# Kernel optimization log

Hardware: AMD Instinct MI355X
Metric: run time of the kernel (lower is better)

The kernel has to match this reference:

```python
import math
import jax, jax.numpy as jnp
import numpy as np
from jax import lax

B, T, D, S, N_SLOTS, N_ITERS = 16, 4096, 768, 768, 16, 8
THR, EPS = 0.5, 1e-8
SCALE = D ** -0.5
NEG = -jnp.finfo(jnp.float32).max


def ln(x, g, b):
    mu = x.mean(-1, keepdims=True)
    var = ((x - mu) ** 2).mean(-1, keepdims=True)
    return (x - mu) / jnp.sqrt(var + 1e-5) * g + b


def gru_cell(u, h, wih, whh, bih, bhh):
    # torch GRUCell: r,z,n gate ordering
    gi = u @ wih.T + bih
    gh = h @ whh.T + bhh
    ir, iz, inn = jnp.split(gi, 3, axis=-1)
    hr, hz, hn = jnp.split(gh, 3, axis=-1)
    r = jax.nn.sigmoid(ir + hr)
    z = jax.nn.sigmoid(iz + hz)
    n = jnp.tanh(inn + r * hn)
    return (1.0 - z) * n + z * h


def sa_step(slots, k, v, p, slot_mask, context_mask):
    q = ln(slots, p['lsg'], p['lsb']) @ p['Wq'].T
    dots = jnp.einsum('bid,bjd->bij', q, k) * SCALE  # [B, n_slots, T]
    dots = jnp.where(context_mask[:, None, :], dots, NEG)
    if slot_mask is not None:
        dots = jnp.where(slot_mask[:, :, None], dots, NEG)
    attn_vis = jax.nn.softmax(dots, axis=1)  # softmax over SLOTS (inverted attn)
    attn = attn_vis + EPS
    attn = attn / attn.sum(-1, keepdims=True)
    updates = jnp.einsum('bjd,bij->bid', v, attn)
    b, n, d = slots.shape
    h = gru_cell(updates.reshape(b * n, d), slots.reshape(b * n, d),
                 p['gwih'], p['gwhh'], p['gbih'], p['gbhh'])
    slots = h.reshape(b, n, d)
    pre = ln(slots, p['lfg'], p['lfb'])
    slots = slots + (jax.nn.relu(pre @ p['w1'].T + p['b1']) @ p['w2'].T + p['b2'])
    return slots, attn_vis


def cluster_single(slots, attn, slot_mask):
    sl = lax.stop_gradient(slots)  # torch no_grad block
    ns = sl / jnp.clip(jnp.linalg.norm(sl, axis=-1, keepdims=True), 1e-12)
    smm = (slot_mask[:, :, None] & slot_mask[:, None, :]).astype(jnp.float32)
    dist = 1.0 - jnp.einsum('bnd,bmd->bnm', ns, ns)
    dist = jnp.where(smm > 0, dist, 2.0)
    adj = (dist < THR).astype(jnp.float32) * smm
    for _ in range(math.ceil(math.log2(N_SLOTS))):  # transitive closure by squaring
        adj = jnp.minimum(adj @ adj, 1.0) * smm
    cum = jnp.cumsum(adj, axis=1)
    cm = adj * (cum <= 1.0)  # keep first row of each connected component
    counts = (cm > 0).any(axis=2).sum(axis=1)
    reset = counts < 3
    eye = jnp.eye(N_SLOTS, dtype=jnp.float32)[None] * slot_mask[:, :, None].astype(jnp.float32)
    cm = jnp.where(reset[:, None, None], eye, cm)
    cw = cm / jnp.clip(cm.sum(axis=2, keepdims=True), 1.0)
    cm = lax.stop_gradient(cm)
    cw = lax.stop_gradient(cw)
    means = cw @ slots          # grads flow through slots only
    cattn = cm @ attn           # grads flow through attn only
    out_mask = (cm > 0).any(axis=2) & slot_mask
    return means, cattn, out_mask


def setup_inputs() -> dict:
    key = jax.random.key(0)
    ks = jax.random.split(key, 16)
    sc = 0.02
    return {
        'x': jax.random.normal(ks[0], (B, T, D), jnp.float32),
        'context_mask': jnp.ones((B, T), jnp.bool_),
        'n_slots': N_SLOTS,
        'slots_init': jax.random.normal(ks[1], (N_SLOTS, S), jnp.float32),
        'Wk': jax.random.normal(ks[2], (S, D), jnp.float32) * sc,
        'Wv': jax.random.normal(ks[3], (S, D), jnp.float32) * sc,
        'Wq': jax.random.normal(ks[4], (S, S), jnp.float32) * sc,
        'gwih': jax.random.normal(ks[5], (3 * S, S), jnp.float32) * sc,
        'gwhh': jax.random.normal(ks[6], (3 * S, S), jnp.float32) * sc,
        'gbih': jnp.zeros((3 * S,), jnp.float32),
        'gbhh': jnp.zeros((3 * S,), jnp.float32),
        'w1': jax.random.normal(ks[7], (4 * S, S), jnp.float32) * sc,
        'b1': jnp.zeros((4 * S,), jnp.float32),
        'w2': jax.random.normal(ks[8], (S, 4 * S), jnp.float32) * sc,
        'b2': jnp.zeros((S,), jnp.float32),
        'lin_g': jnp.ones((D,), jnp.float32), 'lin_b': jnp.zeros((D,), jnp.float32),
        'lsg': jnp.ones((S,), jnp.float32), 'lsb': jnp.zeros((S,), jnp.float32),
        'lfg': jnp.ones((S,), jnp.float32), 'lfb': jnp.zeros((S,), jnp.float32),
    }


def reference(x, context_mask, n_slots, slots_init, Wk, Wv, Wq, gwih, gwhh,
              gbih, gbhh, w1, b1, w2, b2, lin_g, lin_b, lsg, lsb, lfg, lfb):
    p = dict(Wq=Wq, gwih=gwih, gwhh=gwhh, gbih=gbih, gbhh=gbhh,
             w1=w1, b1=b1, w2=w2, b2=b2, lsg=lsg, lsb=lsb, lfg=lfg, lfb=lfb)
    xn = ln(x, lin_g, lin_b)
    init_slots = jnp.broadcast_to(slots_init[None], (x.shape[0], N_SLOTS, S))
    k = xn @ Wk.T
    v = xn @ Wv.T
    slots = init_slots
    for _ in range(N_ITERS):
        slots, attn = sa_step(slots, k, v, p, None, context_mask)
    # implicit differentiation trick
    slots = lax.stop_gradient(slots) - lax.stop_gradient(init_slots) + init_slots
    slot_mask = jnp.ones((x.shape[0], N_SLOTS), jnp.bool_)
    slots, attn = sa_step(slots, k, v, p, slot_mask, context_mask)
    slots, attn, slot_mask = cluster_single(slots, attn, slot_mask)
    attn_map = jnp.transpose(attn, (0, 2, 1))  # [B, T, n_slots]
    return slots, attn_map, slot_mask
```

## Files before the change

kernel.cpp:

```cpp
#include <hip/hip_runtime.h>
#include <hip/hip_bf16.h>

typedef __hip_bfloat16 bf16;
typedef __attribute__((ext_vector_type(4))) float f32x4;
typedef __attribute__((ext_vector_type(8))) short s16x8;
typedef unsigned int u32;
typedef unsigned short u16;

#define B_ 16
#define T_ 4096
#define D_ 768
#define S_ 768
#define NS 16
#define NIT 9
#define NCHUNK 16
#define TCH 256
#define EPS 1e-8f
#define SCALE 0.036084391824351615f

__device__ __forceinline__ void gld16(const void* g, void* l) {
    __builtin_amdgcn_global_load_lds((const __attribute__((address_space(1))) u32*)g,
                                     (__attribute__((address_space(3))) u32*)l, 16, 0, 0);
}

__device__ __forceinline__ u16 bfbits(float x) {
    bf16 h = __float2bfloat16(x);
    return *reinterpret_cast<u16*>(&h);
}

__global__ void __launch_bounds__(256) cvt_all_kernel(
    const float* __restrict__ wq, const float* __restrict__ wk, const float* __restrict__ wv,
    const float* __restrict__ gwih, const float* __restrict__ gwhh,
    const float* __restrict__ w1, const float* __restrict__ w2,
    bf16* __restrict__ wq_b, bf16* __restrict__ wkv_b,
    bf16* __restrict__ gwih_b, bf16* __restrict__ gwhh_b,
    bf16* __restrict__ w1_b, bf16* __restrict__ w2_b)
{
    int i = blockIdx.x * 256 + threadIdx.x;
    const int NW = 589824, NG = 1769472, NM = 2359296;
    if (i < NW) { wq_b[i] = __float2bfloat16(wq[i]); return; }
    i -= NW;
    if (i < NW) { wkv_b[i] = __float2bfloat16(wk[i]); return; }
    i -= NW;
    if (i < NW) { wkv_b[NW + i] = __float2bfloat16(wv[i]); return; }
    i -= NW;
    if (i < NG) { gwih_b[i] = __float2bfloat16(gwih[i]); return; }
    i -= NG;
    if (i < NG) { gwhh_b[i] = __float2bfloat16(gwhh[i]); return; }
    i -= NG;
    if (i < NM) { w1_b[i] = __float2bfloat16(w1[i]); return; }
    i -= NM;
    w2_b[i] = __float2bfloat16(w2[i]);
}

__global__ void __launch_bounds__(256) ln768_kernel(
    const float* __restrict__ x, const float* __restrict__ g,
    const float* __restrict__ bta, bf16* __restrict__ out)
{
    int row = blockIdx.x;
    int tid = threadIdx.x;
    const float* xr = x + (size_t)row * 768;
    float v0 = xr[tid], v1 = xr[tid + 256], v2 = xr[tid + 512];
    float s = v0 + v1 + v2;
    int lane = tid & 63, wid = tid >> 6;
    #pragma unroll
    for (int off = 32; off; off >>= 1) s += __shfl_down(s, off);
    __shared__ float red[4];
    __shared__ float sh_mu, sh_rs;
    if (lane == 0) red[wid] = s;
    __syncthreads();
    if (tid == 0) sh_mu = (red[0] + red[1] + red[2] + red[3]) * (1.f / 768.f);
    __syncthreads();
    float mu = sh_mu;
    float d0 = v0 - mu, d1 = v1 - mu, d2 = v2 - mu;
    float q = d0 * d0 + d1 * d1 + d2 * d2;
    #pragma unroll
    for (int off = 32; off; off >>= 1) q += __shfl_down(q, off);
    if (lane == 0) red[wid] = q;
    __syncthreads();
    if (tid == 0) sh_rs = rsqrtf((red[0] + red[1] + red[2] + red[3]) * (1.f / 768.f) + 1e-5f);
    __syncthreads();
    float rs = sh_rs;
    bf16* orow = out + (size_t)row * 768;
    orow[tid]       = __float2bfloat16(d0 * rs * g[tid]       + bta[tid]);
    orow[tid + 256] = __float2bfloat16(d1 * rs * g[tid + 256] + bta[tid + 256]);
    orow[tid + 512] = __float2bfloat16(d2 * rs * g[tid + 512] + bta[tid + 512]);
}

__global__ void __launch_bounds__(512) gemm256_kernel(
    const bf16* __restrict__ A, const bf16* __restrict__ W,
    bf16* __restrict__ kout, bf16* __restrict__ vTout, float* __restrict__ vsum)
{
    __shared__ char smem[49152];
    __shared__ float vs_l[128];
    bf16* As = (bf16*)smem;
    bf16* Bs = (bf16*)(smem + 32768);
    int tid = threadIdx.x, lane = tid & 63, wid = tid >> 6;
    int bid = blockIdx.x;
    int xcd = bid & 7, idx = bid >> 3;
    int mt = xcd * 32 + idx / 12;
    int nt = idx % 12;
    int bm0 = mt * 256, bn0 = nt * 128;
    int wr = wid >> 1, wc = wid & 1;
    int g = lane >> 4, r15 = lane & 15;
    const f32x4 vzero = {0.f, 0.f, 0.f, 0.f};
    f32x4 acc[4][4];
    #pragma unroll
    for (int m = 0; m < 4; ++m)
        #pragma unroll
        for (int n = 0; n < 4; ++n) acc[m][n] = vzero;

    for (int kt = 0; kt < 768; kt += 64) {
        __syncthreads();
        #pragma unroll
        for (int i = 0; i < 4; ++i) {
            int s0 = i * 512 + wid * 64;
            int o = (s0 + lane) * 16;
            int r = o >> 7, cb = o & 127;
            int cbs = cb ^ ((r & 7) << 4);
            gld16(A + (size_t)(bm0 + r) * 768 + kt + (cbs >> 1), (char*)As + (size_t)s0 * 16);
        }
        #pragma unroll
        for (int i = 0; i < 2; ++i) {
            int s0 = i * 512 + wid * 64;
            int o = (s0 + lane) * 16;
            int r = o >> 7, cb = o & 127;
            int cbs = cb ^ ((r & 7) << 4);
            gld16(W + (size_t)(bn0 + r) * 768 + kt + (cbs >> 1), (char*)Bs + (size_t)s0 * 16);
        }
        asm volatile("s_waitcnt vmcnt(0)" ::: "memory");
        __syncthreads();
        #pragma unroll
        for (int kk2 = 0; kk2 < 2; ++kk2) {
            s16x8 af[4], bfr[4];
            #pragma unroll
            for (int m = 0; m < 4; ++m) {
                int r = wr * 64 + m * 16 + r15;
                int p = r * 128 + ((kk2 * 64 + g * 16) ^ ((r & 7) << 4));
                af[m] = *(const s16x8*)((const char*)As + p);
            }
            #pragma unroll
            for (int n = 0; n < 4; ++n) {
                int r = wc * 64 + n * 16 + r15;
                int p = r * 128 + ((kk2 * 64 + g * 16) ^ ((r & 7) << 4));
                bfr[n] = *(const s16x8*)((const char*)Bs + p);
            }
            #pragma unroll
            for (int m = 0; m < 4; ++m)
                #pragma unroll
                for (int n = 0; n < 4; ++n)
                    acc[m][n] = __builtin_amdgcn_mfma_f32_16x16x32_bf16(af[m], bfr[n], acc[m][n], 0, 0, 0);
        }
    }

    bool is_v = (bn0 >= 768);
    float* Ct = (float*)smem;
    int bq = bm0 >> 12;
    int tloc = bm0 & 4095;
    if (is_v && tid < 128) vs_l[tid] = 0.f;
    #pragma unroll
    for (int q = 0; q < 4; ++q) {
        __syncthreads();
        if (wr == q) {
            #pragma unroll
            for (int m = 0; m < 4; ++m)
                #pragma unroll
                for (int n = 0; n < 4; ++n)
                    #pragma unroll
                    for (int j = 0; j < 4; ++j)
                        Ct[(m * 16 + g * 4 + j) * 132 + wc * 64 + n * 16 + r15] = acc[m][n][j];
        }
        __syncthreads();
        if (!is_v) {
            int r = tid >> 3, cq = tid & 7;
            u16 tmp[16];
            #pragma unroll
            for (int i = 0; i < 16; ++i) tmp[i] = bfbits(Ct[r * 132 + cq * 16 + i]);
            s16x8 o0, o1;
            #pragma unroll
            for (int i = 0; i < 8; ++i) { o0[i] = (short)tmp[i]; o1[i] = (short)tmp[8 + i]; }
            bf16* dst = kout + (size_t)(bm0 + q * 64 + r) * 768 + bn0 + cq * 16;
            *(s16x8*)dst = o0;
            *(s16x8*)(dst + 8) = o1;
        } else {
            int d = tid >> 2, tq = tid & 3;
            float ssum = 0.f;
            u16 tmp[16];
            #pragma unroll
            for (int i = 0; i < 16; ++i) {
                float f = Ct[(tq * 16 + i) * 132 + d];
                ssum += f;
                tmp[i] = bfbits(f);
            }
            s16x8 o0, o1;
            #pragma unroll
            for (int i = 0; i < 8; ++i) { o0[i] = (short)tmp[i]; o1[i] = (short)tmp[8 + i]; }
            bf16* dst = vTout + ((size_t)bq * 768 + (bn0 - 768) + d) * (size_t)T_
                        + tloc + q * 64 + tq * 16;
            *(s16x8*)dst = o0;
            *(s16x8*)(dst + 8) = o1;
            atomicAdd(&vs_l[d], ssum);
        }
    }
    if (is_v) {
        __syncthreads();
        if (tid < 128) atomicAdd(vsum + bq * 768 + (bn0 - 768) + tid, vs_l[tid]);
    }
}

__global__ void init_slots_kernel(const float* __restrict__ si,
                                  float* __restrict__ slots, bf16* __restrict__ slots_bf)
{
    int idx = blockIdx.x * 256 + threadIdx.x;
    float v = si[idx % (NS * S_)];
    slots[idx] = v;
    slots_bf[idx] = __float2bfloat16(v);
}

__global__ void __launch_bounds__(256) ln_gemm_kernel(
    const float* __restrict__ xin, const float* __restrict__ gam, const float* __restrict__ bet,
    const bf16* __restrict__ W, const float* __restrict__ bias,
    bf16* __restrict__ out, int N, int relu)
{
    __shared__ bf16 As[16 * 768];
    __shared__ bf16 Ws[2][64 * 64];
    int tid = threadIdx.x;
    int bx = blockIdx.x, bn0 = blockIdx.y * 64;
    int row = tid >> 4, li = tid & 15;
    const float* xr = xin + (size_t)(bx * 16 + row) * 768;
    float vals[48];
    float s = 0.f;
    #pragma unroll
    for (int i = 0; i < 48; ++i) { vals[i] = xr[li + i * 16]; s += vals[i]; }
    #pragma unroll
    for (int m = 1; m < 16; m <<= 1) s += __shfl_xor(s, m);
    float mu = s * (1.f / 768.f);
    float q = 0.f;
    #pragma unroll
    for (int i = 0; i < 48; ++i) { float d = vals[i] - mu; q += d * d; }
    #pragma unroll
    for (int m = 1; m < 16; m <<= 1) q += __shfl_xor(q, m);
    float rs = rsqrtf(q * (1.f / 768.f) + 1e-5f);
    #pragma unroll
    for (int i = 0; i < 48; ++i) {
        int c = li + i * 16;
        float v = (vals[i] - mu) * rs * gam[c] + bet[c];
        *(u16*)((char*)As + row * 1536 + ((c * 2) ^ ((row & 7) << 4))) = bfbits(v);
    }
    int lane = tid & 63, wid = tid >> 6;
    int g = lane >> 4, s15 = lane & 15;
    auto stageW = [&](int kt, int buf) {
        #pragma unroll
        for (int i = 0; i < 2; ++i) {
            int s0 = i * 256 + wid * 64;
            int o = (s0 + lane) * 16;
            int r = o >> 7, cb = o & 127;
            int cbs = cb ^ ((r & 7) << 4);
            gld16(W + (size_t)(bn0 + r) * 768 + kt + (cbs >> 1),
                  (char*)Ws[buf] + (size_t)s0 * 16);
        }
    };
    stageW(0, 0);
    asm volatile("s_waitcnt vmcnt(0)" ::: "memory");
    __syncthreads();
    f32x4 acc = {0.f, 0.f, 0.f, 0.f};
    int rb = wid * 16 + s15;
    for (int t = 0; t < 12; ++t) {
        int cur = t & 1;
        if (t < 11) stageW((t + 1) * 64, cur ^ 1);
        #pragma unroll
        for (int kk2 = 0; kk2 < 2; ++kk2) {
            int kabs = t * 64 + kk2 * 32;
            s16x8 af = *(const s16x8*)((const char*)As + s15 * 1536 +
                                       ((kabs * 2 + g * 16) ^ ((s15 & 7) << 4)));
            s16x8 bf_ = *(const s16x8*)((const char*)Ws[cur] + rb * 128 +
                                        ((kk2 * 64 + g * 16) ^ ((rb & 7) << 4)));
            acc = __builtin_amdgcn_mfma_f32_16x16x32_bf16(af, bf_, acc, 0, 0, 0);
        }
        asm volatile("s_waitcnt vmcnt(0)" ::: "memory");
        __syncthreads();
    }
    int cn = bn0 + rb;
    float bv = bias ? bias[cn] : 0.f;
    #pragma unroll
    for (int j = 0; j < 4; ++j) {
        float val = acc[j] + bv;
        if (relu) val = fmaxf(val, 0.f);
        out[(size_t)(bx * 16 + g * 4 + j) * N + cn] = __float2bfloat16(val);
    }
}

__device__ __forceinline__ void skinny_body(
    const bf16* A, const bf16* Bm, const float* bias, const float* Cin,
    float* Cf, bf16* Cb, int N, int K, int bm0, int bn0, int relu,
    bf16* As, bf16* Bs)
{
    int tid = threadIdx.x, lane = tid & 63, wid = tid >> 6;
    int g = lane >> 4, r15 = lane & 15;
    f32x4 acc = {0.f, 0.f, 0.f, 0.f};
    for (int kt = 0; kt < K; kt += 64) {
        __syncthreads();
        #pragma unroll
        for (int i = 0; i < 3; ++i) {
            int s0 = i * 256 + wid * 64;
            if (s0 < 640) {
                int o = (s0 + lane) * 16;
                if (o < 2048) {
                    int r = o >> 7, cb = o & 127;
                    int cbs = cb ^ ((r & 7) << 4);
                    gld16(A + (size_t)(bm0 + r) * K + kt + (cbs >> 1), (char*)As + (size_t)s0 * 16);
                } else {
                    int ob = o - 2048;
                    int r = ob >> 7, cb = ob & 127;
                    int cbs = cb ^ ((r & 7) << 4);
                    gld16(Bm + (size_t)(bn0 + r) * K + kt + (cbs >> 1),
                          (char*)Bs + (size_t)(s0 * 16 - 2048));
                }
            }
        }
        asm volatile("s_waitcnt vmcnt(0)" ::: "memory");
        __syncthreads();
        #pragma unroll
        for (int kk = 0; kk < 64; kk += 32) {
            int pa = r15 * 128 + ((kk * 2 + g * 16) ^ ((r15 & 7) << 4));
            s16x8 af = *(const s16x8*)((const char*)As + pa);
            int rb = wid * 16 + r15;
            int pb = rb * 128 + ((kk * 2 + g * 16) ^ ((rb & 7) << 4));
            s16x8 bfr = *(const s16x8*)((const char*)Bs + pb);
            acc = __builtin_amdgcn_mfma_f32_16x16x32_bf16(af, bfr, acc, 0, 0, 0);
        }
    }
    int cn = bn0 + wid * 16 + r15;
    float bv = bias ? bias[cn] : 0.f;
    #pragma unroll
    for (int j = 0; j < 4; ++j) {
        int cm = bm0 + g * 4 + j;
        size_t ci = (size_t)cm * N + cn;
        float val = acc[j] + bv;
        if (Cin) val += Cin[ci];
        if (relu) val = fmaxf(val, 0.f);
        if (Cf) Cf[ci] = val;
        if (Cb) Cb[ci] = __float2bfloat16(val);
    }
}

__global__ void __launch_bounds__(256) mlp2_kernel(
    const bf16* __restrict__ h1, const bf16* __restrict__ W2, const float* __restrict__ b2,
    const float* __restrict__ slotsB, float* __restrict__ slotsA, bf16* __restrict__ slotsA_bf)
{
    __shared__ bf16 As[16 * 64];
    __shared__ bf16 Bs[64 * 64];
    skinny_body(h1, W2, b2, slotsB, slotsA, slotsA_bf, 768, 3072,
                blockIdx.x * 16, blockIdx.y * 64, 0, As, Bs);
}

__global__ void __launch_bounds__(256) gru_gemm_kernel(
    const bf16* __restrict__ upd, const bf16* __restrict__ slots_bf,
    const bf16* __restrict__ Wih, const bf16* __restrict__ Whh,
    const float* __restrict__ bih, const float* __restrict__ bhh,
    float* __restrict__ gi, float* __restrict__ gh)
{
    __shared__ bf16 As[16 * 64];
    __shared__ bf16 Bs[64 * 64];
    int y = blockIdx.y;
    if (y < 36)
        skinny_body(upd, Wih, bih, nullptr, gi, nullptr, 2304, 768,
                    blockIdx.x * 16, y * 64, 0, As, Bs);
    else
        skinny_body(slots_bf, Whh, bhh, nullptr, gh, nullptr, 2304, 768,
                    blockIdx.x * 16, (y - 36) * 64, 0, As, Bs);
}

__global__ void __launch_bounds__(256) fused_attn_kernel(
    const bf16* __restrict__ q_bf, const bf16* __restrict__ k_bf, const bf16* __restrict__ vT,
    float* __restrict__ pU, float* __restrict__ prs, float* __restrict__ avis, int write_avis)
{
    __shared__ char smem[131072];
    bf16* ks0 = (bf16*)smem;
    bf16* ks1 = (bf16*)(smem + 49152);
    bf16* qs  = (bf16*)(smem + 98304);
    char* aL  = smem + 122880;
    __shared__ float rsw[2][16];
    int tid = threadIdx.x, lane = tid & 63, wid = tid >> 6;
    int b = blockIdx.x >> 4, chunk = blockIdx.x & 15;
    int t0 = chunk * TCH;
    int g = lane >> 4, s15 = lane & 15;
    const bf16* qb  = q_bf + (size_t)b * 16 * 768;
    const bf16* kb  = k_bf + (size_t)b * T_ * 768;
    const bf16* vtb = vT + (size_t)b * 768 * T_;

    auto stage_k = [&](int tb, bf16* dst) {
        #pragma unroll
        for (int i = 0; i < 12; ++i) {
            int s0 = i * 256 + wid * 64;
            int o = (s0 + lane) * 16;
            int r = o / 1536, cb = o % 1536;
            int cbs = cb ^ ((r & 7) << 4);
            gld16(kb + (size_t)(tb + r) * 768 + (cbs >> 1), (char*)dst + (size_t)s0 * 16);
        }
    };
    auto stage_v = [&](int tb, bf16* dst) {
        #pragma unroll
        for (int i = 0; i < 12; ++i) {
            int s0 = i * 256 + wid * 64;
            int o = (s0 + lane) * 16;
            int d = o >> 6, cb = o & 63;
            int cbs = cb ^ ((d & 3) << 4);
            gld16(vtb + (size_t)d * T_ + tb + (cbs >> 1), (char*)dst + (size_t)s0 * 16);
        }
    };

    #pragma unroll
    for (int i = 0; i < 6; ++i) {
        int s0 = i * 256 + wid * 64;
        int o = (s0 + lane) * 16;
        int r = o / 1536, cb = o % 1536;
        int cbs = cb ^ ((r & 7) << 4);
        gld16(qb + (size_t)r * 768 + (cbs >> 1), (char*)qs + (size_t)s0 * 16);
    }
    stage_k(t0, ks0);
    asm volatile("s_waitcnt vmcnt(0)" ::: "memory");
    __syncthreads();

    const f32x4 vzero = {0.f, 0.f, 0.f, 0.f};
    float rs_acc = 0.f;

    for (int ts = 0; ts < 8; ++ts) {
        bf16* cur = (ts & 1) ? ks1 : ks0;
        bf16* nxt = (ts & 1) ? ks0 : ks1;
        if (ts < 7) stage_k(t0 + (ts + 1) * 32, nxt);
        if (wid < 2) {
            f32x4 dacc = vzero;
            #pragma unroll
            for (int kk = 0; kk < 768; kk += 32) {
                int rk = wid * 16 + s15;
                int pk = rk * 1536 + ((kk * 2 + g * 16) ^ ((rk & 7) << 4));
                s16x8 kf = *(const s16x8*)((const char*)cur + pk);
                int pq = s15 * 1536 + ((kk * 2 + g * 16) ^ ((s15 & 7) << 4));
                s16x8 qf = *(const s16x8*)((const char*)qs + pq);
                dacc = __builtin_amdgcn_mfma_f32_16x16x32_bf16(kf, qf, dacc, 0, 0, 0);
            }
            float d0 = dacc[0] * SCALE, d1 = dacc[1] * SCALE,
                  d2 = dacc[2] * SCALE, d3 = dacc[3] * SCALE;
            float m0 = d0, m1 = d1, m2 = d2, m3 = d3;
            #pragma unroll
            for (int off = 1; off < 16; off <<= 1) {
                m0 = fmaxf(m0, __shfl_xor(m0, off));
                m1 = fmaxf(m1, __shfl_xor(m1, off));
                m2 = fmaxf(m2, __shfl_xor(m2, off));
                m3 = fmaxf(m3, __shfl_xor(m3, off));
            }
            float e0 = expf(d0 - m0), e1 = expf(d1 - m1), e2 = expf(d2 - m2), e3 = expf(d3 - m3);
            float q0 = e0, q1 = e1, q2 = e2, q3 = e3;
            #pragma unroll
            for (int off = 1; off < 16; off <<= 1) {
                q0 += __shfl_xor(q0, off);
                q1 += __shfl_xor(q1, off);
                q2 += __shfl_xor(q2, off);
                q3 += __shfl_xor(q3, off);
            }
            float a0 = e0 / q0, a1 = e1 / q1, a2 = e2 / q2, a3 = e3 / q3;
            rs_acc += a0 + a1 + a2 + a3;
            int tl = wid * 16 + g * 4;
            ushort2 p0, p1;
            p0.x = bfbits(a0); p0.y = bfbits(a1);
            p1.x = bfbits(a2); p1.y = bfbits(a3);
            int sw = (s15 & 3) << 4;
            char* aS = aL + ts * 1024;
            *(ushort2*)(aS + s15 * 64 + ((tl * 2) ^ sw))       = p0;
            *(ushort2*)(aS + s15 * 64 + (((tl + 2) * 2) ^ sw)) = p1;
            if (write_avis) {
                f32x4 w = {a0, a1, a2, a3};
                *(f32x4*)(avis + (size_t)(b * 16 + s15) * T_ + t0 + ts * 32 + tl) = w;
            }
        }
        asm volatile("s_waitcnt vmcnt(0)" ::: "memory");
        __syncthreads();
    }

    f32x4 uacc[12];
    #pragma unroll
    for (int i = 0; i < 12; ++i) uacc[i] = vzero;
    stage_v(t0, ks0);
    asm volatile("s_waitcnt vmcnt(0)" ::: "memory");
    __syncthreads();
    for (int ts = 0; ts < 8; ++ts) {
        bf16* cur = (ts & 1) ? ks1 : ks0;
        bf16* nxt = (ts & 1) ? ks0 : ks1;
        if (ts < 7) stage_v(t0 + (ts + 1) * 32, nxt);
        {
            int pa = ts * 1024 + s15 * 64 + ((g * 16) ^ ((s15 & 3) << 4));
            s16x8 afr = *(const s16x8*)(aL + pa);
            #pragma unroll
            for (int i = 0; i < 12; ++i) {
                int d = (wid * 12 + i) * 16 + s15;
                int pv = d * 64 + ((g * 16) ^ ((d & 3) << 4));
                s16x8 vf = *(const s16x8*)((const char*)cur + pv);
                uacc[i] = __builtin_amdgcn_mfma_f32_16x16x32_bf16(vf, afr, uacc[i], 0, 0, 0);
            }
        }
        asm volatile("s_waitcnt vmcnt(0)" ::: "memory");
        __syncthreads();
    }

    float* pUb = pU + (size_t)(b * 16 + chunk) * 768 * 16;
    #pragma unroll
    for (int i = 0; i < 12; ++i) {
        int dbase = (wid * 12 + i) * 16 + g * 4;
        #pragma unroll
        for (int j = 0; j < 4; ++j)
            pUb[(size_t)(dbase + j) * 16 + s15] = uacc[i][j];
    }
    rs_acc += __shfl_xor(rs_acc, 16);
    rs_acc += __shfl_xor(rs_acc, 32);
    if (wid < 2 && lane < 16) rsw[wid][s15] = rs_acc;
    __syncthreads();
    if (tid < 16) prs[(b * 16 + chunk) * 16 + tid] = rsw[0][tid] + rsw[1][tid];
}

__global__ void __launch_bounds__(256) attn_reduce_kernel(
    const float* __restrict__ pU, const float* __restrict__ prs,
    const float* __restrict__ vsum, bf16* __restrict__ upd)
{
    int idx = blockIdx.x * 256 + threadIdx.x;
    int d = idx % 768;
    int s = (idx / 768) & 15;
    int b = idx / (768 * 16);
    float su = 0.f;
    #pragma unroll
    for (int c = 0; c < 16; ++c) su += pU[((size_t)(b * 16 + c) * 768 + d) * 16 + s];
    float rs = 0.f;
    #pragma unroll
    for (int c = 0; c < 16; ++c) rs += prs[(b * 16 + c) * 16 + s];
    float val = (su + EPS * vsum[b * 768 + d]) / (rs + T_ * EPS);
    upd[idx] = __float2bfloat16(val);
}

__global__ void __launch_bounds__(256) gru_gates_kernel(
    const float* __restrict__ gi, const float* __restrict__ gh,
    const float* __restrict__ slotsA, float* __restrict__ slotsB)
{
    int idx = blockIdx.x * 256 + threadIdx.x;
    int r = idx / 768, c = idx - r * 768;
    const float* gir = gi + (size_t)r * 2304;
    const float* ghr = gh + (size_t)r * 2304;
    float ir = gir[c], iz = gir[768 + c], inn = gir[1536 + c];
    float hr = ghr[c], hz = ghr[768 + c], hn  = ghr[1536 + c];
    float rg = 1.f / (1.f + expf(-(ir + hr)));
    float z  = 1.f / (1.f + expf(-(iz + hz)));
    float n  = tanhf(inn + rg * hn);
    float h  = slotsA[idx];
    slotsB[idx] = (1.f - z) * n + z * h;
}

__global__ void __launch_bounds__(256) cluster_kernel(
    const float* __restrict__ slots, float* __restrict__ out_slots,
    float* __restrict__ out_mask, float* __restrict__ cm_g)
{
    int b = blockIdx.x;
    __shared__ float s[16][768];
    __shared__ float inv[16];
    __shared__ float adj[16][16], tmp[16][16], cw[16][16];
    __shared__ int reset_s;
    const float* sb = slots + (size_t)b * 16 * 768;
    for (int i = threadIdx.x; i < 16 * 768; i += 256) s[i / 768][i % 768] = sb[i];
    __syncthreads();
    if (threadIdx.x < 16) {
        float q = 0.f;
        for (int d = 0; d < 768; ++d) q += s[threadIdx.x][d] * s[threadIdx.x][d];
        inv[threadIdx.x] = 1.f / fmaxf(sqrtf(q), 1e-12f);
    }
    __syncthreads();
    int n = threadIdx.x >> 4, m = threadIdx.x & 15;
    float dot = 0.f;
    for (int d = 0; d < 768; ++d) dot += s[n][d] * s[m][d];
    dot *= inv[n] * inv[m];
    adj[n][m] = ((1.f - dot) < 0.5f) ? 1.f : 0.f;
    __syncthreads();
    #pragma unroll
    for (int it = 0; it < 4; ++it) {
        float t = 0.f;
        #pragma unroll
        for (int j = 0; j < 16; ++j) t += adj[n][j] * adj[j][m];
        tmp[n][m] = fminf(t, 1.f);
        __syncthreads();
        adj[n][m] = tmp[n][m];
        __syncthreads();
    }
    if (threadIdx.x < 16) {
        int mm = threadIdx.x;
        float run = 0.f;
        for (int nn = 0; nn < 16; ++nn) {
            run += adj[nn][mm];
            tmp[nn][mm] = adj[nn][mm] * ((run <= 1.f) ? 1.f : 0.f);
        }
    }
    __syncthreads();
    if (threadIdx.x == 0) {
        int cnt = 0;
        for (int nn = 0; nn < 16; ++nn) {
            bool any = false;
            for (int j = 0; j < 16; ++j) any = any || (tmp[nn][j] > 0.f);
            cnt += any ? 1 : 0;
        }
        reset_s = (cnt < 3) ? 1 : 0;
    }
    __syncthreads();
    if (reset_s) tmp[n][m] = (n == m) ? 1.f : 0.f;
    __syncthreads();
    if (threadIdx.x < 16) {
        float rs = 0.f;
        for (int j = 0; j < 16; ++j) rs += tmp[threadIdx.x][j];
        rs = fmaxf(rs, 1.f);
        for (int j = 0; j < 16; ++j) cw[threadIdx.x][j] = tmp[threadIdx.x][j] / rs;
        bool any = false;
        for (int j = 0; j < 16; ++j) any = any || (tmp[threadIdx.x][j] > 0.f);
        out_mask[b * 16 + threadIdx.x] = any ? 1.f : 0.f;
    }
    cm_g[b * 256 + threadIdx.x] = tmp[n][m];
    __syncthreads();
    for (int i = threadIdx.x; i < 16 * 768; i += 256) {
        int nn = i / 768, d = i - nn * 768;
        float acc = 0.f;
        #pragma unroll
        for (int j = 0; j < 16; ++j) acc += cw[nn][j] * s[j][d];
        out_slots[(size_t)b * 16 * 768 + i] = acc;
    }
}

__global__ void __launch_bounds__(256) cattn_kernel(
    const float* __restrict__ av, const float* __restrict__ cm_g, float* __restrict__ out_attn)
{
    int b = blockIdx.y;
    int t = blockIdx.x * 256 + threadIdx.x;
    __shared__ float cm[16][16];
    cm[threadIdx.x >> 4][threadIdx.x & 15] = cm_g[b * 256 + threadIdx.x];
    __syncthreads();
    float avv[16];
    #pragma unroll
    for (int j = 0; j < 16; ++j) avv[j] = av[((size_t)b * 16 + j) * T_ + t];
    #pragma unroll
    for (int i = 0; i < 16; ++i) {
        float acc = 0.f;
        #pragma unroll
        for (int j = 0; j < 16; ++j) acc += cm[i][j] * avv[j];
        out_attn[((size_t)b * T_ + t) * 16 + i] = acc;
    }
}

extern "C" void kernel_launch(void* const* d_in, const int* in_sizes, int n_in,
                              void* d_out, int out_size, void* d_ws, size_t ws_size,
                              hipStream_t stream)
{
    const float* x    = (const float*)d_in[0];
    const float* si   = (const float*)d_in[3];
    const float* Wk   = (const float*)d_in[4];
    const float* Wv   = (const float*)d_in[5];
    const float* Wq   = (const float*)d_in[6];
    const float* gwih = (const float*)d_in[7];
    const float* gwhh = (const float*)d_in[8];
    const float* gbih = (const float*)d_in[9];
    const float* gbhh = (const float*)d_in[10];
    const float* w1   = (const float*)d_in[11];
    const float* b1   = (const float*)d_in[12];
    const float* w2   = (const float*)d_in[13];
    const float* b2   = (const float*)d_in[14];
    const float* ling = (const float*)d_in[15];
    const float* linb = (const float*)d_in[16];
    const float* lsg  = (const float*)d_in[17];
    const float* lsb  = (const float*)d_in[18];
    const float* lfg  = (const float*)d_in[19];
    const float* lfb  = (const float*)d_in[20];

    char* w = (char*)d_ws;
    size_t off = 0;
    auto alloc = [&](size_t bytes) { void* p = w + off; off += (bytes + 255) & ~(size_t)255; return p; };
    bf16* xn     = (bf16*)alloc((size_t)B_ * T_ * D_ * 2);
    bf16* k_bf   = (bf16*)alloc((size_t)B_ * T_ * S_ * 2);
    bf16* vT     = (bf16*)alloc((size_t)B_ * S_ * T_ * 2);
    float* avis  = (float*)alloc((size_t)B_ * NS * T_ * 4);
    float* pU    = (float*)alloc((size_t)B_ * NCHUNK * S_ * NS * 4);
    float* prs   = (float*)alloc((size_t)B_ * NCHUNK * NS * 4);
    float* vsum  = (float*)alloc((size_t)B_ * S_ * 4);
    float* slotsA = (float*)alloc((size_t)B_ * NS * S_ * 4);
    bf16* slotsA_bf = (bf16*)alloc((size_t)B_ * NS * S_ * 2);
    float* slotsB = (float*)alloc((size_t)B_ * NS * S_ * 4);
    bf16* q_bf   = (bf16*)alloc((size_t)B_ * NS * S_ * 2);
    bf16* upd_bf = (bf16*)alloc((size_t)B_ * NS * S_ * 2);
    float* gi    = (float*)alloc((size_t)B_ * NS * 3 * S_ * 4);
    float* gh    = (float*)alloc((size_t)B_ * NS * 3 * S_ * 4);
    bf16* h1_bf  = (bf16*)alloc((size_t)B_ * NS * 4 * S_ * 2);
    bf16* wq_bf  = (bf16*)alloc((size_t)S_ * S_ * 2);
    bf16* wkv_bf = (bf16*)alloc((size_t)1536 * D_ * 2);
    bf16* gwih_bf = (bf16*)alloc((size_t)3 * S_ * S_ * 2);
    bf16* gwhh_bf = (bf16*)alloc((size_t)3 * S_ * S_ * 2);
    bf16* w1_bf  = (bf16*)alloc((size_t)4 * S_ * S_ * 2);
    bf16* w2_bf  = (bf16*)alloc((size_t)S_ * 4 * S_ * 2);
    float* cm_g  = (float*)alloc((size_t)B_ * 256 * 4);

    float* out_slots = (float*)d_out;
    float* out_attn  = out_slots + (size_t)B_ * NS * S_;
    float* out_mask  = out_attn + (size_t)B_ * T_ * NS;

    cvt_all_kernel<<<39168, 256, 0, stream>>>(Wq, Wk, Wv, gwih, gwhh, w1, w2,
                                              wq_bf, wkv_bf, gwih_bf, gwhh_bf, w1_bf, w2_bf);

    ln768_kernel<<<B_ * T_, 256, 0, stream>>>(x, ling, linb, xn);

    (void)hipMemsetAsync(vsum, 0, (size_t)B_ * S_ * 4, stream);
    gemm256_kernel<<<3072, 512, 0, stream>>>(xn, wkv_bf, k_bf, vT, vsum);

    init_slots_kernel<<<(B_ * NS * S_) / 256, 256, 0, stream>>>(si, slotsA, slotsA_bf);

    for (int it = 0; it < NIT; ++it) {
        {
            dim3 g(16, 12);
            ln_gemm_kernel<<<g, 256, 0, stream>>>(slotsA, lsg, lsb, wq_bf, nullptr,
                                                  q_bf, 768, 0);
        }
        fused_attn_kernel<<<B_ * NCHUNK, 256, 0, stream>>>(q_bf, k_bf, vT, pU, prs, avis,
                                                           (it == NIT - 1) ? 1 : 0);
        attn_reduce_kernel<<<(B_ * NS * S_) / 256, 256, 0, stream>>>(pU, prs, vsum, upd_bf);
        {
            dim3 g(16, 72);
            gru_gemm_kernel<<<g, 256, 0, stream>>>(upd_bf, slotsA_bf, gwih_bf, gwhh_bf,
                                                   gbih, gbhh, gi, gh);
        }
        gru_gates_kernel<<<(B_ * NS * S_) / 256, 256, 0, stream>>>(gi, gh, slotsA, slotsB);
        {
            dim3 g(16, 48);
            ln_gemm_kernel<<<g, 256, 0, stream>>>(slotsB, lfg, lfb, w1_bf, b1,
                                                  h1_bf, 3072, 1);
        }
        {
            dim3 g(16, 12);
            mlp2_kernel<<<g, 256, 0, stream>>>(h1_bf, w2_bf, b2, slotsB, slotsA, slotsA_bf);
        }
    }

    cluster_kernel<<<B_, 256, 0, stream>>>(slotsA, out_slots, out_mask, cm_g);
    {
        dim3 g(T_ / 256, B_);
        cattn_kernel<<<g, 256, 0, stream>>>(avis, cm_g, out_attn);
    }
}
```

Baseline: 1.464 ms.

## Fuse slot-attention iteration loop into one persistent cooperative kernel with grid syncs

```diff
diff --git a/kernel.cpp b/kernel.cpp
--- a/kernel.cpp
+++ b/kernel.cpp
@@ -1,5 +1,8 @@
 #include <hip/hip_runtime.h>
 #include <hip/hip_bf16.h>
+#include <hip/hip_cooperative_groups.h>
+
+namespace cg = cooperative_groups;
 
 typedef __hip_bfloat16 bf16;
 typedef __attribute__((ext_vector_type(4))) float f32x4;
@@ -175,7 +178,11 @@
             int r = tid >> 3, cq = tid & 7;
             u16 tmp[16];
             #pragma unroll
-            for (int i = 0; i < 16; ++i) tmp[i] = bfbits(Ct[r * 132 + cq * 16 + i]);
+            for (int i = 0; i < 4; ++i) {
+                f32x4 vv = *(const f32x4*)&Ct[r * 132 + cq * 16 + i * 4];
+                #pragma unroll
+                for (int jj = 0; jj < 4; ++jj) tmp[i * 4 + jj] = bfbits(vv[jj]);
+            }
             s16x8 o0, o1;
             #pragma unroll
             for (int i = 0; i < 8; ++i) { o0[i] = (short)tmp[i]; o1[i] = (short)tmp[8 + i]; }
@@ -217,16 +224,14 @@
     slots_bf[idx] = __float2bfloat16(v);
 }
 
-__global__ void __launch_bounds__(256) ln_gemm_kernel(
-    const float* __restrict__ xin, const float* __restrict__ gam, const float* __restrict__ bet,
-    const bf16* __restrict__ W, const float* __restrict__ bias,
-    bf16* __restrict__ out, int N, int relu)
-{
-    __shared__ bf16 As[16 * 768];
-    __shared__ bf16 Ws[2][64 * 64];
-    int tid = threadIdx.x;
-    int bx = blockIdx.x, bn0 = blockIdx.y * 64;
-    int row = tid >> 4, li = tid & 15;
+
+__device__ __forceinline__ void ln_gemm_body(
+    int htid, const float* __restrict__ xin, const float* __restrict__ gam,
+    const float* __restrict__ bet, const bf16* __restrict__ W, const float* __restrict__ bias,
+    bf16* __restrict__ out, int N, int relu, int bx, int bn0, bool act, char* sm)
+{
+    bf16* As = (bf16*)sm;
+    int row = htid >> 4, li = htid & 15;
     const float* xr = xin + (size_t)(bx * 16 + row) * 768;
     float vals[48];
     float s = 0.f;
@@ -247,24 +252,24 @@
         float v = (vals[i] - mu) * rs * gam[c] + bet[c];
         *(u16*)((char*)As + row * 1536 + ((c * 2) ^ ((row & 7) << 4))) = bfbits(v);
     }
-    int lane = tid & 63, wid = tid >> 6;
+    int lane = htid & 63, hw = htid >> 6;
     int g = lane >> 4, s15 = lane & 15;
     auto stageW = [&](int kt, int buf) {
         #pragma unroll
         for (int i = 0; i < 2; ++i) {
-            int s0 = i * 256 + wid * 64;
+            int s0 = i * 256 + hw * 64;
             int o = (s0 + lane) * 16;
             int r = o >> 7, cb = o & 127;
             int cbs = cb ^ ((r & 7) << 4);
             gld16(W + (size_t)(bn0 + r) * 768 + kt + (cbs >> 1),
-                  (char*)Ws[buf] + (size_t)s0 * 16);
+                  sm + 24576 + buf * 8192 + (size_t)s0 * 16);
         }
     };
     stageW(0, 0);
     asm volatile("s_waitcnt vmcnt(0)" ::: "memory");
     __syncthreads();
     f32x4 acc = {0.f, 0.f, 0.f, 0.f};
-    int rb = wid * 16 + s15;
+    int rb = hw * 16 + s15;
     for (int t = 0; t < 12; ++t) {
         int cur = t & 1;
         if (t < 11) stageW((t + 1) * 64, cur ^ 1);
@@ -273,36 +278,41 @@
             int kabs = t * 64 + kk2 * 32;
             s16x8 af = *(const s16x8*)((const char*)As + s15 * 1536 +
                                        ((kabs * 2 + g * 16) ^ ((s15 & 7) << 4)));
-            s16x8 bf_ = *(const s16x8*)((const char*)Ws[cur] + rb * 128 +
+            s16x8 bf_ = *(const s16x8*)(sm + 24576 + cur * 8192 + rb * 128 +
                                         ((kk2 * 64 + g * 16) ^ ((rb & 7) << 4)));
             acc = __builtin_amdgcn_mfma_f32_16x16x32_bf16(af, bf_, acc, 0, 0, 0);
         }
         asm volatile("s_waitcnt vmcnt(0)" ::: "memory");
         __syncthreads();
     }
-    int cn = bn0 + rb;
-    float bv = bias ? bias[cn] : 0.f;
-    #pragma unroll
-    for (int j = 0; j < 4; ++j) {
-        float val = acc[j] + bv;
-        if (relu) val = fmaxf(val, 0.f);
-        out[(size_t)(bx * 16 + g * 4 + j) * N + cn] = __float2bfloat16(val);
-    }
-}
-
-__device__ __forceinline__ void skinny_body(
-    const bf16* A, const bf16* Bm, const float* bias, const float* Cin,
-    float* Cf, bf16* Cb, int N, int K, int bm0, int bn0, int relu,
-    bf16* As, bf16* Bs)
-{
-    int tid = threadIdx.x, lane = tid & 63, wid = tid >> 6;
+    if (act) {
+        int cn = bn0 + rb;
+        float bv = bias ? bias[cn] : 0.f;
+        #pragma unroll
+        for (int j = 0; j < 4; ++j) {
+            float val = acc[j] + bv;
+            if (relu) val = fmaxf(val, 0.f);
+            out[(size_t)(bx * 16 + g * 4 + j) * N + cn] = __float2bfloat16(val);
+        }
+    }
+}
+
+__device__ __forceinline__ void skinny_body2(
+    int htid, const bf16* __restrict__ A, const bf16* __restrict__ Bm,
+    const float* __restrict__ bias, const float* __restrict__ Cin,
+    float* __restrict__ Cf, bf16* __restrict__ Cb, int N, int K,
+    int bm0, int bn0, int relu, bool act, char* sm)
+{
+    bf16* As = (bf16*)sm;
+    bf16* Bs = (bf16*)(sm + 2048);
+    int lane = htid & 63, hw = htid >> 6;
     int g = lane >> 4, r15 = lane & 15;
     f32x4 acc = {0.f, 0.f, 0.f, 0.f};
     for (int kt = 0; kt < K; kt += 64) {
         __syncthreads();
         #pragma unroll
         for (int i = 0; i < 3; ++i) {
-            int s0 = i * 256 + wid * 64;
+            int s0 = i * 256 + hw * 64;
             if (s0 < 640) {
                 int o = (s0 + lane) * 16;
                 if (o < 2048) {
@@ -324,75 +334,50 @@
         for (int kk = 0; kk < 64; kk += 32) {
             int pa = r15 * 128 + ((kk * 2 + g * 16) ^ ((r15 & 7) << 4));
             s16x8 af = *(const s16x8*)((const char*)As + pa);
-            int rb = wid * 16 + r15;
+            int rb = hw * 16 + r15;
             int pb = rb * 128 + ((kk * 2 + g * 16) ^ ((rb & 7) << 4));
             s16x8 bfr = *(const s16x8*)((const char*)Bs + pb);
             acc = __builtin_amdgcn_mfma_f32_16x16x32_bf16(af, bfr, acc, 0, 0, 0);
         }
     }
-    int cn = bn0 + wid * 16 + r15;
-    float bv = bias ? bias[cn] : 0.f;
-    #pragma unroll
-    for (int j = 0; j < 4; ++j) {
-        int cm = bm0 + g * 4 + j;
-        size_t ci = (size_t)cm * N + cn;
-        float val = acc[j] + bv;
-        if (Cin) val += Cin[ci];
-        if (relu) val = fmaxf(val, 0.f);
-        if (Cf) Cf[ci] = val;
-        if (Cb) Cb[ci] = __float2bfloat16(val);
-    }
-}
-
-__global__ void __launch_bounds__(256) mlp2_kernel(
-    const bf16* __restrict__ h1, const bf16* __restrict__ W2, const float* __restrict__ b2,
-    const float* __restrict__ slotsB, float* __restrict__ slotsA, bf16* __restrict__ slotsA_bf)
-{
-    __shared__ bf16 As[16 * 64];
-    __shared__ bf16 Bs[64 * 64];
-    skinny_body(h1, W2, b2, slotsB, slotsA, slotsA_bf, 768, 3072,
-                blockIdx.x * 16, blockIdx.y * 64, 0, As, Bs);
-}
-
-__global__ void __launch_bounds__(256) gru_gemm_kernel(
-    const bf16* __restrict__ upd, const bf16* __restrict__ slots_bf,
-    const bf16* __restrict__ Wih, const bf16* __restrict__ Whh,
-    const float* __restrict__ bih, const float* __restrict__ bhh,
-    float* __restrict__ gi, float* __restrict__ gh)
-{
-    __shared__ bf16 As[16 * 64];
-    __shared__ bf16 Bs[64 * 64];
-    int y = blockIdx.y;
-    if (y < 36)
-        skinny_body(upd, Wih, bih, nullptr, gi, nullptr, 2304, 768,
-                    blockIdx.x * 16, y * 64, 0, As, Bs);
-    else
-        skinny_body(slots_bf, Whh, bhh, nullptr, gh, nullptr, 2304, 768,
-                    blockIdx.x * 16, (y - 36) * 64, 0, As, Bs);
-}
-
-__global__ void __launch_bounds__(256) fused_attn_kernel(
-    const bf16* __restrict__ q_bf, const bf16* __restrict__ k_bf, const bf16* __restrict__ vT,
-    float* __restrict__ pU, float* __restrict__ prs, float* __restrict__ avis, int write_avis)
-{
-    __shared__ char smem[131072];
+    __syncthreads();
+    if (act) {
+        int cn = bn0 + hw * 16 + r15;
+        float bv = bias ? bias[cn] : 0.f;
+        #pragma unroll
+        for (int j = 0; j < 4; ++j) {
+            int cm = bm0 + g * 4 + j;
+            size_t ci = (size_t)cm * N + cn;
+            float val = acc[j] + bv;
+            if (Cin) val += Cin[ci];
+            if (relu) val = fmaxf(val, 0.f);
+            if (Cf) Cf[ci] = val;
+            if (Cb) Cb[ci] = __float2bfloat16(val);
+        }
+    }
+}
+
+__device__ __forceinline__ void attn_body(
+    int tid, int blk, const bf16* __restrict__ q_bf, const bf16* __restrict__ k_bf,
+    const bf16* __restrict__ vT, float* __restrict__ pU, float* __restrict__ prs,
+    float* __restrict__ avis, int write_avis, char* smem, float (*rsw)[16])
+{
     bf16* ks0 = (bf16*)smem;
     bf16* ks1 = (bf16*)(smem + 49152);
     bf16* qs  = (bf16*)(smem + 98304);
     char* aL  = smem + 122880;
-    __shared__ float rsw[2][16];
-    int tid = threadIdx.x, lane = tid & 63, wid = tid >> 6;
-    int b = blockIdx.x >> 4, chunk = blockIdx.x & 15;
+    int lane = tid & 63, wid = tid >> 6;
+    int b = blk >> 4, chunk = blk & 15;
     int t0 = chunk * TCH;
     int g = lane >> 4, s15 = lane & 15;
     const bf16* qb  = q_bf + (size_t)b * 16 * 768;
     const bf16* kb  = k_bf + (size_t)b * T_ * 768;
-    const bf16* vtb = vT + (size_t)b * 768 * T_;
+    const bf16* vtb = vT + (size_t)b * 768 * (size_t)T_;
 
     auto stage_k = [&](int tb, bf16* dst) {
         #pragma unroll
-        for (int i = 0; i < 12; ++i) {
-            int s0 = i * 256 + wid * 64;
+        for (int i = 0; i < 6; ++i) {
+            int s0 = i * 512 + wid * 64;
             int o = (s0 + lane) * 16;
             int r = o / 1536, cb = o % 1536;
             int cbs = cb ^ ((r & 7) << 4);
@@ -401,8 +386,8 @@
     };
     auto stage_v = [&](int tb, bf16* dst) {
         #pragma unroll
-        for (int i = 0; i < 12; ++i) {
-            int s0 = i * 256 + wid * 64;
+        for (int i = 0; i < 6; ++i) {
+            int s0 = i * 512 + wid * 64;
             int o = (s0 + lane) * 16;
             int d = o >> 6, cb = o & 63;
             int cbs = cb ^ ((d & 3) << 4);
@@ -411,8 +396,8 @@
     };
 
     #pragma unroll
-    for (int i = 0; i < 6; ++i) {
-        int s0 = i * 256 + wid * 64;
+    for (int i = 0; i < 3; ++i) {
+        int s0 = i * 512 + wid * 64;
         int o = (s0 + lane) * 16;
         int r = o / 1536, cb = o % 1536;
         int cbs = cb ^ ((r & 7) << 4);
@@ -470,17 +455,17 @@
             *(ushort2*)(aS + s15 * 64 + ((tl * 2) ^ sw))       = p0;
             *(ushort2*)(aS + s15 * 64 + (((tl + 2) * 2) ^ sw)) = p1;
             if (write_avis) {
-                f32x4 w = {a0, a1, a2, a3};
-                *(f32x4*)(avis + (size_t)(b * 16 + s15) * T_ + t0 + ts * 32 + tl) = w;
+                f32x4 wv = {a0, a1, a2, a3};
+                *(f32x4*)(avis + (size_t)(b * 16 + s15) * T_ + t0 + ts * 32 + tl) = wv;
             }
         }
         asm volatile("s_waitcnt vmcnt(0)" ::: "memory");
         __syncthreads();
     }
 
-    f32x4 uacc[12];
-    #pragma unroll
-    for (int i = 0; i < 12; ++i) uacc[i] = vzero;
+    f32x4 uacc[6];
+    #pragma unroll
+    for (int i = 0; i < 6; ++i) uacc[i] = vzero;
     stage_v(t0, ks0);
     asm volatile("s_waitcnt vmcnt(0)" ::: "memory");
     __syncthreads();
@@ -492,8 +477,8 @@
             int pa = ts * 1024 + s15 * 64 + ((g * 16) ^ ((s15 & 3) << 4));
             s16x8 afr = *(const s16x8*)(aL + pa);
             #pragma unroll
-            for (int i = 0; i < 12; ++i) {
-                int d = (wid * 12 + i) * 16 + s15;
+            for (int i = 0; i < 6; ++i) {
+                int d = (wid * 6 + i) * 16 + s15;
                 int pv = d * 64 + ((g * 16) ^ ((d & 3) << 4));
                 s16x8 vf = *(const s16x8*)((const char*)cur + pv);
                 uacc[i] = __builtin_amdgcn_mfma_f32_16x16x32_bf16(vf, afr, uacc[i], 0, 0, 0);
@@ -505,8 +490,8 @@
 
     float* pUb = pU + (size_t)(b * 16 + chunk) * 768 * 16;
     #pragma unroll
-    for (int i = 0; i < 12; ++i) {
-        int dbase = (wid * 12 + i) * 16 + g * 4;
+    for (int i = 0; i < 6; ++i) {
+        int dbase = (wid * 6 + i) * 16 + g * 4;
         #pragma unroll
         for (int j = 0; j < 4; ++j)
             pUb[(size_t)(dbase + j) * 16 + s15] = uacc[i][j];
@@ -518,39 +503,101 @@
     if (tid < 16) prs[(b * 16 + chunk) * 16 + tid] = rsw[0][tid] + rsw[1][tid];
 }
 
-__global__ void __launch_bounds__(256) attn_reduce_kernel(
-    const float* __restrict__ pU, const float* __restrict__ prs,
-    const float* __restrict__ vsum, bf16* __restrict__ upd)
-{
-    int idx = blockIdx.x * 256 + threadIdx.x;
-    int d = idx % 768;
-    int s = (idx / 768) & 15;
-    int b = idx / (768 * 16);
-    float su = 0.f;
-    #pragma unroll
-    for (int c = 0; c < 16; ++c) su += pU[((size_t)(b * 16 + c) * 768 + d) * 16 + s];
-    float rs = 0.f;
-    #pragma unroll
-    for (int c = 0; c < 16; ++c) rs += prs[(b * 16 + c) * 16 + s];
-    float val = (su + EPS * vsum[b * 768 + d]) / (rs + T_ * EPS);
-    upd[idx] = __float2bfloat16(val);
-}
-
-__global__ void __launch_bounds__(256) gru_gates_kernel(
-    const float* __restrict__ gi, const float* __restrict__ gh,
-    const float* __restrict__ slotsA, float* __restrict__ slotsB)
-{
-    int idx = blockIdx.x * 256 + threadIdx.x;
-    int r = idx / 768, c = idx - r * 768;
-    const float* gir = gi + (size_t)r * 2304;
-    const float* ghr = gh + (size_t)r * 2304;
-    float ir = gir[c], iz = gir[768 + c], inn = gir[1536 + c];
-    float hr = ghr[c], hz = ghr[768 + c], hn  = ghr[1536 + c];
-    float rg = 1.f / (1.f + expf(-(ir + hr)));
-    float z  = 1.f / (1.f + expf(-(iz + hz)));
-    float n  = tanhf(inn + rg * hn);
-    float h  = slotsA[idx];
-    slotsB[idx] = (1.f - z) * n + z * h;
+__global__ void __launch_bounds__(512) sa_loop_kernel(
+    const bf16* __restrict__ k_bf, const bf16* __restrict__ vT, const float* __restrict__ vsum,
+    float* __restrict__ slotsA, bf16* __restrict__ slotsA_bf, float* __restrict__ slotsB,
+    bf16* __restrict__ q_bf, bf16* __restrict__ upd_bf,
+    float* __restrict__ gi, float* __restrict__ gh, bf16* __restrict__ h1_bf,
+    float* __restrict__ pU, float* __restrict__ prs, float* __restrict__ avis,
+    const bf16* __restrict__ wq, const bf16* __restrict__ wih, const bf16* __restrict__ whh,
+    const float* __restrict__ bih, const float* __restrict__ bhh,
+    const bf16* __restrict__ w1, const float* __restrict__ b1,
+    const bf16* __restrict__ w2, const float* __restrict__ b2,
+    const float* __restrict__ lsg, const float* __restrict__ lsb,
+    const float* __restrict__ lfg, const float* __restrict__ lfb)
+{
+    __shared__ char smem[131072];
+    __shared__ float rsw[2][16];
+    cg::grid_group grid = cg::this_grid();
+    int tid = threadIdx.x, blk = blockIdx.x;
+    int h = tid >> 8, htid = tid & 255;
+    int w = blk * 2 + h;
+
+    for (int it = 0; it < NIT; ++it) {
+        {
+            bool act = w < 192;
+            int t = act ? w : 0;
+            ln_gemm_body(htid, slotsA, lsg, lsb, wq, nullptr, q_bf, 768, 0,
+                         t & 15, (t >> 4) * 64, act, smem + h * 40960);
+        }
+        grid.sync();
+        attn_body(tid, blk, q_bf, k_bf, vT, pU, prs, avis,
+                  (it == NIT - 1) ? 1 : 0, smem, rsw);
+        grid.sync();
+        #pragma unroll
+        for (int i = 0; i < 2; ++i) {
+            int idx = blk * 512 + tid + i * 131072;
+            if (idx < 196608) {
+                int d = idx % 768, sl = (idx / 768) & 15, bb = idx / 12288;
+                float su = 0.f;
+                #pragma unroll
+                for (int c = 0; c < 16; ++c)
+                    su += pU[((size_t)(bb * 16 + c) * 768 + d) * 16 + sl];
+                float rsum = 0.f;
+                #pragma unroll
+                for (int c = 0; c < 16; ++c)
+                    rsum += prs[(bb * 16 + c) * 16 + sl];
+                upd_bf[idx] = __float2bfloat16((su + EPS * vsum[bb * 768 + d]) / (rsum + T_ * EPS));
+            }
+        }
+        grid.sync();
+        for (int i = 0; i < 3; ++i) {
+            int t = w + i * 512;
+            bool act = t < 1152;
+            if (!act) t = 0;
+            int bx = t & 15, y = t >> 4;
+            bool ih = y < 36;
+            const bf16* Am_ = ih ? upd_bf : slotsA_bf;
+            const bf16* Bw_ = ih ? wih : whh;
+            const float* bias_ = ih ? bih : bhh;
+            float* out_ = ih ? gi : gh;
+            int bn0 = (ih ? y : y - 36) * 64;
+            skinny_body2(htid, Am_, Bw_, bias_, nullptr, out_, nullptr, 2304, 768,
+                         bx * 16, bn0, 0, act, smem + h * 10240);
+        }
+        grid.sync();
+        #pragma unroll
+        for (int i = 0; i < 2; ++i) {
+            int idx = blk * 512 + tid + i * 131072;
+            if (idx < 196608) {
+                int r = idx / 768, c = idx - r * 768;
+                const float* gir = gi + (size_t)r * 2304;
+                const float* ghr = gh + (size_t)r * 2304;
+                float ir = gir[c], iz = gir[768 + c], inn = gir[1536 + c];
+                float hr = ghr[c], hz = ghr[768 + c], hn = ghr[1536 + c];
+                float rg = 1.f / (1.f + expf(-(ir + hr)));
+                float z  = 1.f / (1.f + expf(-(iz + hz)));
+                float n  = tanhf(inn + rg * hn);
+                slotsB[idx] = (1.f - z) * n + z * slotsA[idx];
+            }
+        }
+        grid.sync();
+        for (int i = 0; i < 2; ++i) {
+            int t = w + i * 512;
+            bool act = t < 768;
+            if (!act) t = 0;
+            ln_gemm_body(htid, slotsB, lfg, lfb, w1, b1, h1_bf, 3072, 1,
+                         t & 15, (t >> 4) * 64, act, smem + h * 40960);
+        }
+        grid.sync();
+        {
+            bool act = w < 192;
+            int t = act ? w : 0;
+            skinny_body2(htid, h1_bf, w2, b2, slotsB, slotsA, slotsA_bf, 768, 3072,
+                         (t & 15) * 16, (t >> 4) * 64, 0, act, smem + h * 10240);
+        }
+        grid.sync();
+    }
 }
 
 __global__ void __launch_bounds__(256) cluster_kernel(
@@ -712,30 +759,19 @@
 
     init_slots_kernel<<<(B_ * NS * S_) / 256, 256, 0, stream>>>(si, slotsA, slotsA_bf);
 
-    for (int it = 0; it < NIT; ++it) {
-        {
-            dim3 g(16, 12);
-            ln_gemm_kernel<<<g, 256, 0, stream>>>(slotsA, lsg, lsb, wq_bf, nullptr,
-                                                  q_bf, 768, 0);
-        }
-        fused_attn_kernel<<<B_ * NCHUNK, 256, 0, stream>>>(q_bf, k_bf, vT, pU, prs, avis,
-                                                           (it == NIT - 1) ? 1 : 0);
-        attn_reduce_kernel<<<(B_ * NS * S_) / 256, 256, 0, stream>>>(pU, prs, vsum, upd_bf);
-        {
-            dim3 g(16, 72);
-            gru_gemm_kernel<<<g, 256, 0, stream>>>(upd_bf, slotsA_bf, gwih_bf, gwhh_bf,
-                                                   gbih, gbhh, gi, gh);
-        }
-        gru_gates_kernel<<<(B_ * NS * S_) / 256, 256, 0, stream>>>(gi, gh, slotsA, slotsB);
-        {
-            dim3 g(16, 48);
-            ln_gemm_kernel<<<g, 256, 0, stream>>>(slotsB, lfg, lfb, w1_bf, b1,
-                                                  h1_bf, 3072, 1);
-        }
-        {
-            dim3 g(16, 12);
-            mlp2_kernel<<<g, 256, 0, stream>>>(h1_bf, w2_bf, b2, slotsB, slotsA, slotsA_bf);
-        }
+    {
+        void* args[] = {
+            (void*)&k_bf, (void*)&vT, (void*)&vsum,
+            (void*)&slotsA, (void*)&slotsA_bf, (void*)&slotsB,
+            (void*)&q_bf, (void*)&upd_bf, (void*)&gi, (void*)&gh, (void*)&h1_bf,
+            (void*)&pU, (void*)&prs, (void*)&avis,
+            (void*)&wq_bf, (void*)&gwih_bf, (void*)&gwhh_bf,
+            (void*)&gbih, (void*)&gbhh,
+            (void*)&w1_bf, (void*)&b1, (void*)&w2_bf, (void*)&b2,
+            (void*)&lsg, (void*)&lsb, (void*)&lfg, (void*)&lfb
+        };
+        (void)hipLaunchCooperativeKernel((const void*)sa_loop_kernel,
+                                         dim3(256), dim3(512), args, 0, stream);
     }
 
     cluster_kernel<<<B_, 256, 0, stream>>>(slotsA, out_slots, out_mask, cm_g);
```

After: 4.684 ms. 220% more time.
